# Optimization experiments

Hardware: AMD Instinct MI355X
Metric: run time of the kernel (lower is better)

## Reference

```python
import jax, jax.numpy as jnp
import numpy as np

N = 100_000      # num nodes
R = 7            # num relations
D = 64           # input_dim == output_dim
E = 1_600_000    # num edges
EDIM = 16        # edge_input_dim


def setup_inputs() -> dict:
    key = jax.random.key(0)
    ks = jax.random.split(key, 10)
    node_in = jax.random.randint(ks[0], (E,), 0, N)
    node_out = jax.random.randint(ks[1], (E,), 0, N)
    relation = jax.random.randint(ks[2], (E,), 0, R)
    edge_list = jnp.stack([node_in, node_out, relation], axis=1)  # (E, 3)
    x = jax.random.normal(ks[3], (N, D), dtype=jnp.float32)
    edge_weight = jax.random.uniform(ks[4], (E,), dtype=jnp.float32)
    edge_feature = jax.random.normal(ks[5], (E, EDIM), dtype=jnp.float32)
    s = 1.0 / np.sqrt(R * D)
    W_lin = jax.random.uniform(ks[6], (D, R * D), minval=-s, maxval=s, dtype=jnp.float32)
    b_lin = jnp.zeros((D,), jnp.float32)
    s2 = 1.0 / np.sqrt(D)
    W_self = jax.random.uniform(ks[7], (D, D), minval=-s2, maxval=s2, dtype=jnp.float32)
    b_self = jnp.zeros((D,), jnp.float32)
    s3 = 1.0 / np.sqrt(EDIM)
    W_edge = jax.random.uniform(ks[8], (D, EDIM), minval=-s3, maxval=s3, dtype=jnp.float32)
    b_edge = jnp.zeros((D,), jnp.float32)
    return {"x": x, "edge_list": edge_list, "edge_weight": edge_weight,
            "edge_feature": edge_feature, "W_lin": W_lin, "b_lin": b_lin,
            "W_self": W_self, "b_self": b_self, "W_edge": W_edge, "b_edge": b_edge}


def reference(x, edge_list, edge_weight, edge_feature, W_lin, b_lin, W_self, b_self, W_edge, b_edge):
    node_in, node_out, relation = edge_list[:, 0], edge_list[:, 1], edge_list[:, 2]
    # destination index in the flattened (node, relation) space
    seg = node_out * R + relation  # (E,)
    # sparse.mm(adj.T, x): scatter w * x[src] into (N*R, D)
    msg = edge_weight[:, None] * x[node_in]  # (E, D)
    update = jax.ops.segment_sum(msg, seg, num_segments=N * R)  # (N*R, D)
    # edge feature branch: edge_linear then weighted scatter_add
    edge_msg = (edge_feature @ W_edge.T + b_edge) * edge_weight[:, None]  # (E, D)
    update = update + jax.ops.segment_sum(edge_msg, seg, num_segments=N * R)
    update = update.reshape(N, R * D)
    out = update @ W_lin.T + b_lin + x @ W_self.T + b_self
    return jax.nn.relu(out)
```

## Files before the change

kernel.cpp:

```cpp
#include <hip/hip_runtime.h>
#include <hip/hip_bf16.h>
#include <hip/hip_fp16.h>

#define N_NODES 100000
#define R_REL   7
#define E_EDGES 1600000
#define EDIM    16
#define KTOT    640
#define AROWB   1280
#define CAP     56
#define CSTR    16

#define ASWZ(row, cb) ((row) * AROWB + ((cb) ^ (((row) & 7) << 4)))

typedef __bf16 bf16_t;
typedef bf16_t bf16x8 __attribute__((ext_vector_type(8)));
typedef bf16_t bf16x4 __attribute__((ext_vector_type(4)));
typedef float  f32x4  __attribute__((ext_vector_type(4)));
typedef unsigned long long u64;

#define RFL(v) __builtin_amdgcn_readfirstlane(v)
#define RL(v, l) __builtin_amdgcn_readlane(v, l)


__global__ __launch_bounds__(256) void k_pre(
    const float* __restrict__ x, const int* __restrict__ el,
    const float* __restrict__ wgt,
    const float* __restrict__ W_lin, const float* __restrict__ W_self,
    const float* __restrict__ W_edge, const float* __restrict__ b_edge,
    int* __restrict__ cnt, bf16_t* __restrict__ xb, bf16_t* __restrict__ Bp,
    u64* __restrict__ recs8)
{
    const int t = blockIdx.x * 256 + threadIdx.x;

    if (t < (N_NODES * 64) / 16) {
        const float4* xp = (const float4*)(x + (size_t)t * 16);
        float4 v0 = xp[0], v1 = xp[1], v2 = xp[2], v3 = xp[3];
        bf16x8 o0 = {(bf16_t)v0.x, (bf16_t)v0.y, (bf16_t)v0.z, (bf16_t)v0.w,
                     (bf16_t)v1.x, (bf16_t)v1.y, (bf16_t)v1.z, (bf16_t)v1.w};
        bf16x8 o1 = {(bf16_t)v2.x, (bf16_t)v2.y, (bf16_t)v2.z, (bf16_t)v2.w,
                     (bf16_t)v3.x, (bf16_t)v3.y, (bf16_t)v3.z, (bf16_t)v3.w};
        *(bf16x8*)(xb + (size_t)t * 16)     = o0;
        *(bf16x8*)(xb + (size_t)t * 16 + 8) = o1;
    }

    if (t < KTOT * 64) {
        int k = t >> 6;
        int j = t & 63;
        float v;
        if (k < 448) {
            v = W_lin[j * 448 + k];
        } else if (k < 512) {
            v = W_self[j * 64 + (k - 448)];
        } else if (k < 624) {
            int r = (k - 512) >> 4, kk = (k - 512) & 15;
            float sacc = 0.f;
            for (int d = 0; d < 64; d++)
                sacc = fmaf(W_lin[j * 448 + r * 64 + d], W_edge[d * 16 + kk], sacc);
            v = sacc;
        } else if (k < 631) {
            int r = k - 624;
            float sacc = 0.f;
            for (int d = 0; d < 64; d++)
                sacc = fmaf(W_lin[j * 448 + r * 64 + d], b_edge[d], sacc);
            v = sacc;
        } else {
            v = 0.f;
        }
        Bp[((k >> 3) * 64 + j) * 8 + (k & 7)] = (bf16_t)v;
    }

    if (t < E_EDGES / 4) {
        const int4* ep = (const int4*)(el + (size_t)t * 12);
        int4 q0 = ep[0], q1 = ep[1], q2 = ep[2];
        float4 w4 = *(const float4*)(wgt + (size_t)t * 4);
        const int e = t * 4;
        const int srcs[4] = {q0.x, q0.w, q1.z, q2.y};
        const int dsts[4] = {q0.y, q1.x, q1.w, q2.z};
        const int rels[4] = {q0.z, q1.y, q2.x, q2.w};
        const float ws[4] = {w4.x, w4.y, w4.z, w4.w};
        int slot[4];
#pragma unroll
        for (int i = 0; i < 4; i++)
            slot[i] = atomicAdd(&cnt[dsts[i] * CSTR], 1);
#pragma unroll
        for (int i = 0; i < 4; i++) {
            unsigned u0 = (unsigned)srcs[i] | ((unsigned)rels[i] << 17)
                        | ((unsigned)((e + i) & 0xFFF) << 20);
            unsigned u1 = ((unsigned)(e + i) >> 12)
                        | (__float_as_uint(ws[i]) & 0xFFFFFE00u);
            recs8[(size_t)dsts[i] * CAP + slot[i]] = ((u64)u1 << 32) | u0;
        }
    }
}


__global__ __launch_bounds__(256, 8) void k_main(
    const bf16_t* __restrict__ xb, const float* __restrict__ ef,
    const float* __restrict__ b_lin, const float* __restrict__ b_self,
    const int* __restrict__ cnt, const u64* __restrict__ recs8,
    const bf16_t* __restrict__ Bp, float* __restrict__ out)
{
    __shared__ __align__(16) unsigned char A[16 * AROWB];
    const int wave = threadIdx.x >> 6;
    const int lane = threadIdx.x & 63;
    const int lef  = lane & 15;
    const int nodeBase = blockIdx.x * 16;
    const int n0 = nodeBase + wave * 4;

    int    md[4];
    u64    rw[4];
    bf16_t sv[4];
#pragma unroll
    for (int i = 0; i < 4; i++) {
        md[i] = min(cnt[(n0 + i) * CSTR], CAP);
        rw[i] = (lane < md[i]) ? recs8[(size_t)(n0 + i) * CAP + lane] : 0ull;
        sv[i] = xb[(n0 + i) * 64 + lane];
    }

#pragma unroll
    for (int i = 0; i < 4; i++) {
        const int row = wave * 4 + i;
        *(bf16_t*)(A + ASWZ(row, (448 + lane) * 2)) = sv[i];
        if (lane < 9) *(bf16_t*)(A + ASWZ(row, (631 + lane) * 2)) = (bf16_t)0.f;

        const int m = md[i];
        const unsigned u0v = (unsigned)rw[i];
        const unsigned u1v = (unsigned)(rw[i] >> 32);
        const int  relv  = (u0v >> 17) & 7;
        const bool valid = lane < m;

        for (int r = 0; r < R_REL; r++) {
            u64 mr = __ballot(valid && (relv == r));
            float a = 0.f, F = 0.f, s = 0.f;
            while (mr) {
                int i0 = __builtin_ctzll(mr); mr &= mr - 1;
                unsigned a0 = RL(u0v, i0), b0 = RL(u1v, i0);
                int src0 = a0 & 0x1FFFF;
                int e0 = (a0 >> 20) | ((b0 & 0x1FF) << 12);
                float w0 = __uint_as_float(b0 & 0xFFFFFE00u);
                float xv0 = (float)xb[src0 * 64 + lane];
                float ev0 = ef[e0 * EDIM + lef];
                if (mr) {
                    int i1 = __builtin_ctzll(mr); mr &= mr - 1;
                    unsigned a1 = RL(u0v, i1), b1 = RL(u1v, i1);
                    int src1 = a1 & 0x1FFFF;
                    int e1 = (a1 >> 20) | ((b1 & 0x1FF) << 12);
                    float w1 = __uint_as_float(b1 & 0xFFFFFE00u);
                    float xv1 = (float)xb[src1 * 64 + lane];
                    float ev1 = ef[e1 * EDIM + lef];
                    if (mr) {
                        int i2 = __builtin_ctzll(mr); mr &= mr - 1;
                        int i3 = i2; bool four = false;
                        if (mr) { i3 = __builtin_ctzll(mr); mr &= mr - 1; four = true; }
                        unsigned a2 = RL(u0v, i2), b2 = RL(u1v, i2);
                        unsigned a3 = RL(u0v, i3), b3 = RL(u1v, i3);
                        int src2 = a2 & 0x1FFFF, src3 = a3 & 0x1FFFF;
                        int e2 = (a2 >> 20) | ((b2 & 0x1FF) << 12);
                        int e3 = (a3 >> 20) | ((b3 & 0x1FF) << 12);
                        float w2 = __uint_as_float(b2 & 0xFFFFFE00u);
                        float w3 = four ? __uint_as_float(b3 & 0xFFFFFE00u) : 0.f;
                        float xv2 = (float)xb[src2 * 64 + lane];
                        float xv3 = (float)xb[src3 * 64 + lane];
                        float ev2 = ef[e2 * EDIM + lef];
                        float ev3 = ef[e3 * EDIM + lef];
                        a = fmaf(w2, xv2, a); F = fmaf(w2, ev2, F); s += w2;
                        a = fmaf(w3, xv3, a); F = fmaf(w3, ev3, F); s += w3;
                    }
                    a = fmaf(w1, xv1, a); F = fmaf(w1, ev1, F); s += w1;
                }
                a = fmaf(w0, xv0, a); F = fmaf(w0, ev0, F); s += w0;
            }
            *(bf16_t*)(A + ASWZ(row, (r * 64 + lane) * 2)) = (bf16_t)a;
            if (lane < EDIM)
                *(bf16_t*)(A + ASWZ(row, (512 + r * EDIM + lane) * 2)) = (bf16_t)F;
            if (lane == 0)
                *(bf16_t*)(A + ASWZ(row, (624 + r) * 2)) = (bf16_t)s;
        }
    }
    __syncthreads();

    const int quad = lane >> 4;
    const int l15  = lane & 15;
    const unsigned abase = (unsigned)l15 * AROWB;
    const unsigned aswz  = (unsigned)((l15 & 7) << 4);
    f32x4 c = {0.f, 0.f, 0.f, 0.f};
#pragma unroll
    for (int s2i = 0; s2i < KTOT / 32; s2i++) {
        bf16x8 a = *(const bf16x8*)(A + abase
                     + (((unsigned)(s2i * 64 + quad * 16)) ^ aswz));
        bf16x8 b = *(const bf16x8*)(Bp + (((s2i * 4 + quad) * 64) + wave * 16 + l15) * 8);
        c = __builtin_amdgcn_mfma_f32_16x16x32_bf16(a, b, c, 0, 0, 0);
    }
    const int j = wave * 16 + l15;
    const float bias = b_lin[j] + b_self[j];
#pragma unroll
    for (int q = 0; q < 4; q++) {
        const int n = nodeBase + quad * 4 + q;
        float v = c[q] + bias;
        out[n * 64 + j] = v > 0.f ? v : 0.f;
    }
}


extern "C" void kernel_launch(void* const* d_in, const int* in_sizes, int n_in,
                              void* d_out, int out_size, void* d_ws, size_t ws_size,
                              hipStream_t stream) {
    const float* x      = (const float*)d_in[0];
    const int*   el     = (const int*)  d_in[1];
    const float* wgt    = (const float*)d_in[2];
    const float* ef     = (const float*)d_in[3];
    const float* W_lin  = (const float*)d_in[4];
    const float* b_lin  = (const float*)d_in[5];
    const float* W_self = (const float*)d_in[6];
    const float* b_self = (const float*)d_in[7];
    const float* W_edge = (const float*)d_in[8];
    const float* b_edge = (const float*)d_in[9];
    float* out = (float*)d_out;

    u64*    recs8 = (u64*)d_ws;
    int*    cnt   = (int*)(recs8 + (size_t)N_NODES * CAP);
    bf16_t* xb    = (bf16_t*)(cnt + (size_t)N_NODES * CSTR);
    bf16_t* Bp    = xb + (size_t)N_NODES * 64;

    hipMemsetAsync(cnt, 0, (size_t)N_NODES * CSTR * sizeof(int), stream);
    k_pre <<<1563, 256, 0, stream>>>(x, el, wgt, W_lin, W_self, W_edge, b_edge,
                                     cnt, xb, Bp, recs8);
    k_main<<<N_NODES / 16, 256, 0, stream>>>(xb, ef, b_lin, b_self,
                                             cnt, recs8, Bp, out);
}
```

Baseline: 380.9 us.

## Sort edges by relation in-wave and gather in batched chunks of sixteen

Instead of looping over 7 relations with a ballot and a dependent 1-4 deep gather chain each, the kernel computes a per-lane rank by relation using ballots, popcount prefix sums and mbcnt. It then permutes the edge records into relation order with ds_permute and issues up to 16 independent x/ef gathers per chunk before accumulating, flushing a relation's sums whenever the relation changes. The A tile is zero-filled up front so empty relations need no stores, and nodes with no edges are skipped. Occupancy hint is lowered from 8 to 6 to give room for the larger register footprint of the 16-wide gather batch.

Result: slower. 546.4 us (+43.4%).

```diff
diff --git a/kernel.cpp b/kernel.cpp
--- a/kernel.cpp
+++ b/kernel.cpp
@@ -10,12 +10,12 @@
 #define AROWB   1280
 #define CAP     56
 #define CSTR    16
+#define CHUNK   16
 
 #define ASWZ(row, cb) ((row) * AROWB + ((cb) ^ (((row) & 7) << 4)))
 
 typedef __bf16 bf16_t;
 typedef bf16_t bf16x8 __attribute__((ext_vector_type(8)));
-typedef bf16_t bf16x4 __attribute__((ext_vector_type(4)));
 typedef float  f32x4  __attribute__((ext_vector_type(4)));
 typedef unsigned long long u64;
 
@@ -95,7 +95,7 @@
 }
 
 
-__global__ __launch_bounds__(256, 8) void k_main(
+__global__ __launch_bounds__(256, 6) void k_main(
     const bf16_t* __restrict__ xb, const float* __restrict__ ef,
     const float* __restrict__ b_lin, const float* __restrict__ b_self,
     const int* __restrict__ cnt, const u64* __restrict__ recs8,
@@ -108,75 +108,102 @@
     const int nodeBase = blockIdx.x * 16;
     const int n0 = nodeBase + wave * 4;
 
-    int    md[4];
-    u64    rw[4];
-    bf16_t sv[4];
-#pragma unroll
-    for (int i = 0; i < 4; i++) {
-        md[i] = min(cnt[(n0 + i) * CSTR], CAP);
-        rw[i] = (lane < md[i]) ? recs8[(size_t)(n0 + i) * CAP + lane] : 0ull;
-        sv[i] = xb[(n0 + i) * 64 + lane];
-    }
-
+    int md[4];
+    u64 rw[4];
 #pragma unroll
     for (int i = 0; i < 4; i++) {
         const int row = wave * 4 + i;
-        *(bf16_t*)(A + ASWZ(row, (448 + lane) * 2)) = sv[i];
-        if (lane < 9) *(bf16_t*)(A + ASWZ(row, (631 + lane) * 2)) = (bf16_t)0.f;
-
+        md[i] = RFL(min(cnt[(n0 + i) * CSTR], CAP));
+        rw[i] = (lane < md[i]) ? recs8[(size_t)(n0 + i) * CAP + lane] : 0ull;
+        *(bf16_t*)(A + ASWZ(row, (448 + lane) * 2)) = xb[(n0 + i) * 64 + lane];
+        uint4 z = {0u, 0u, 0u, 0u};
+        if (lane < 56) *(uint4*)(A + ASWZ(row, lane * 16)) = z;
+        if (lane < 16) *(uint4*)(A + ASWZ(row, 1024 + lane * 16)) = z;
+    }
+
+#pragma unroll
+    for (int i = 0; i < 4; i++) {
+        const int row = wave * 4 + i;
         const int m = md[i];
-        const unsigned u0v = (unsigned)rw[i];
-        const unsigned u1v = (unsigned)(rw[i] >> 32);
-        const int  relv  = (u0v >> 17) & 7;
+        if (m == 0) continue;
+        const int u0v = (int)(unsigned)rw[i];
+        const int u1v = (int)(unsigned)(rw[i] >> 32);
+        const int relv = ((unsigned)u0v >> 17) & 7;
         const bool valid = lane < m;
 
-        for (int r = 0; r < R_REL; r++) {
-            u64 mr = __ballot(valid && (relv == r));
-            float a = 0.f, F = 0.f, s = 0.f;
-            while (mr) {
-                int i0 = __builtin_ctzll(mr); mr &= mr - 1;
-                unsigned a0 = RL(u0v, i0), b0 = RL(u1v, i0);
-                int src0 = a0 & 0x1FFFF;
-                int e0 = (a0 >> 20) | ((b0 & 0x1FF) << 12);
-                float w0 = __uint_as_float(b0 & 0xFFFFFE00u);
-                float xv0 = (float)xb[src0 * 64 + lane];
-                float ev0 = ef[e0 * EDIM + lef];
-                if (mr) {
-                    int i1 = __builtin_ctzll(mr); mr &= mr - 1;
-                    unsigned a1 = RL(u0v, i1), b1 = RL(u1v, i1);
-                    int src1 = a1 & 0x1FFFF;
-                    int e1 = (a1 >> 20) | ((b1 & 0x1FF) << 12);
-                    float w1 = __uint_as_float(b1 & 0xFFFFFE00u);
-                    float xv1 = (float)xb[src1 * 64 + lane];
-                    float ev1 = ef[e1 * EDIM + lef];
-                    if (mr) {
-                        int i2 = __builtin_ctzll(mr); mr &= mr - 1;
-                        int i3 = i2; bool four = false;
-                        if (mr) { i3 = __builtin_ctzll(mr); mr &= mr - 1; four = true; }
-                        unsigned a2 = RL(u0v, i2), b2 = RL(u1v, i2);
-                        unsigned a3 = RL(u0v, i3), b3 = RL(u1v, i3);
-                        int src2 = a2 & 0x1FFFF, src3 = a3 & 0x1FFFF;
-                        int e2 = (a2 >> 20) | ((b2 & 0x1FF) << 12);
-                        int e3 = (a3 >> 20) | ((b3 & 0x1FF) << 12);
-                        float w2 = __uint_as_float(b2 & 0xFFFFFE00u);
-                        float w3 = four ? __uint_as_float(b3 & 0xFFFFFE00u) : 0.f;
-                        float xv2 = (float)xb[src2 * 64 + lane];
-                        float xv3 = (float)xb[src3 * 64 + lane];
-                        float ev2 = ef[e2 * EDIM + lef];
-                        float ev3 = ef[e3 * EDIM + lef];
-                        a = fmaf(w2, xv2, a); F = fmaf(w2, ev2, F); s += w2;
-                        a = fmaf(w3, xv3, a); F = fmaf(w3, ev3, F); s += w3;
+        u64 g0 = __ballot(valid && relv == 0);
+        u64 g1 = __ballot(valid && relv == 1);
+        u64 g2 = __ballot(valid && relv == 2);
+        u64 g3 = __ballot(valid && relv == 3);
+        u64 g4 = __ballot(valid && relv == 4);
+        u64 g5 = __ballot(valid && relv == 5);
+        u64 g6 = __ballot(valid && relv == 6);
+        const int c0 = __builtin_popcountll(g0), c1 = __builtin_popcountll(g1);
+        const int c2 = __builtin_popcountll(g2), c3 = __builtin_popcountll(g3);
+        const int c4 = __builtin_popcountll(g4), c5 = __builtin_popcountll(g5);
+        const int p0 = 0, p1 = c0, p2 = p1 + c1, p3 = p2 + c2;
+        const int p4 = p3 + c3, p5 = p4 + c4, p6 = p5 + c5;
+        const bool b0 = relv & 1, b1 = relv & 2, b2 = relv & 4;
+        u64 t0 = b0 ? g1 : g0, t1 = b0 ? g3 : g2, t2 = b0 ? g5 : g4, t3 = g6;
+        u64 sA = b1 ? t1 : t0, sB = b1 ? t3 : t2;
+        u64 mm = b2 ? sB : sA;
+        int pa = b0 ? p1 : p0, pb = b0 ? p3 : p2, pc = b0 ? p5 : p4, pd = p6;
+        int pe_ = b1 ? pb : pa, pf_ = b1 ? pd : pc;
+        int pfx = b2 ? pf_ : pe_;
+        int rig = __builtin_amdgcn_mbcnt_hi((unsigned)(mm >> 32),
+                  __builtin_amdgcn_mbcnt_lo((unsigned)mm, 0));
+        int rank = valid ? (pfx + rig) : lane;
+        const int su0 = __builtin_amdgcn_ds_permute(rank * 4, u0v);
+        const int su1 = __builtin_amdgcn_ds_permute(rank * 4, u1v);
+
+        float a = 0.f, F = 0.f, sw_ = 0.f;
+        int cur = -1;
+        int base = 0;
+        while (base < m) {
+            const int nk = min(m - base, CHUNK);
+            unsigned short xv[CHUNK];
+            float ev[CHUNK], wk[CHUNK];
+            int rk[CHUNK];
+#pragma unroll
+            for (int k = 0; k < CHUNK; k++) {
+                if (k < nk) {
+                    const int uu0 = RL(su0, base + k);
+                    const int uu1 = RL(su1, base + k);
+                    const int src = uu0 & 0x1FFFF;
+                    const int e   = (int)(((unsigned)uu0) >> 20)
+                                  | ((uu1 & 0x1FF) << 12);
+                    rk[k] = (int)((((unsigned)uu0) >> 17) & 7);
+                    wk[k] = __uint_as_float((unsigned)uu1 & 0xFFFFFE00u);
+                    xv[k] = *(const unsigned short*)(xb + ((size_t)src << 6) + lane);
+                    ev[k] = ef[(size_t)e * EDIM + lef];
+                }
+            }
+#pragma unroll
+            for (int k = 0; k < CHUNK; k++) {
+                if (k < nk) {
+                    if (rk[k] != cur) {
+                        if (cur >= 0) {
+                            *(bf16_t*)(A + ASWZ(row, (cur * 64 + lane) * 2)) = (bf16_t)a;
+                            if (lane < EDIM)
+                                *(bf16_t*)(A + ASWZ(row, (512 + cur * EDIM + lane) * 2)) = (bf16_t)F;
+                            if (lane == 0)
+                                *(bf16_t*)(A + ASWZ(row, (624 + cur) * 2)) = (bf16_t)sw_;
+                        }
+                        a = 0.f; F = 0.f; sw_ = 0.f; cur = rk[k];
                     }
-                    a = fmaf(w1, xv1, a); F = fmaf(w1, ev1, F); s += w1;
+                    const float xf = __uint_as_float(((unsigned)xv[k]) << 16);
+                    a   = fmaf(wk[k], xf,    a);
+                    F   = fmaf(wk[k], ev[k], F);
+                    sw_ += wk[k];
                 }
-                a = fmaf(w0, xv0, a); F = fmaf(w0, ev0, F); s += w0;
             }
-            *(bf16_t*)(A + ASWZ(row, (r * 64 + lane) * 2)) = (bf16_t)a;
-            if (lane < EDIM)
-                *(bf16_t*)(A + ASWZ(row, (512 + r * EDIM + lane) * 2)) = (bf16_t)F;
-            if (lane == 0)
-                *(bf16_t*)(A + ASWZ(row, (624 + r) * 2)) = (bf16_t)s;
+            base += nk;
         }
+        *(bf16_t*)(A + ASWZ(row, (cur * 64 + lane) * 2)) = (bf16_t)a;
+        if (lane < EDIM)
+            *(bf16_t*)(A + ASWZ(row, (512 + cur * EDIM + lane) * 2)) = (bf16_t)F;
+        if (lane == 0)
+            *(bf16_t*)(A + ASWZ(row, (624 + cur) * 2)) = (bf16_t)sw_;
     }
     __syncthreads();
 
@@ -187,10 +214,10 @@
     f32x4 c = {0.f, 0.f, 0.f, 0.f};
 #pragma unroll
     for (int s2i = 0; s2i < KTOT / 32; s2i++) {
-        bf16x8 a = *(const bf16x8*)(A + abase
+        bf16x8 av = *(const bf16x8*)(A + abase
                      + (((unsigned)(s2i * 64 + quad * 16)) ^ aswz));
-        bf16x8 b = *(const bf16x8*)(Bp + (((s2i * 4 + quad) * 64) + wave * 16 + l15) * 8);
-        c = __builtin_amdgcn_mfma_f32_16x16x32_bf16(a, b, c, 0, 0, 0);
+        bf16x8 bv = *(const bf16x8*)(Bp + (((s2i * 4 + quad) * 64) + wave * 16 + l15) * 8);
+        c = __builtin_amdgcn_mfma_f32_16x16x32_bf16(av, bv, c, 0, 0, 0);
     }
     const int j = wave * 16 + l15;
     const float bias = b_lin[j] + b_self[j];
```
